# Performance work log

Measured on AMD Instinct MI355X. Metric: run time of the kernel, lower is better.

## Reference

```python
import jax, jax.numpy as jnp
import numpy as np

H, W, C = 64, 64, 64
B = 64
N_HEADS = 4
CONV_FILTERS = 64
BASIS_DIM = 16


def get_spatial_basis(h, w, d):
    half_d = d // 2
    basis = np.zeros((h, w, d), dtype=np.float32)
    div = np.exp(np.arange(0, half_d, 2, dtype=np.float32) * -np.log(100.0) / half_d)
    h_grid = np.expand_dims(np.arange(0, h, dtype=np.float32), 1)
    w_grid = np.expand_dims(np.arange(0, w, dtype=np.float32), 1)
    basis[:, :, 0:half_d:2] = np.sin(h_grid * div)[:, np.newaxis, :]
    basis[:, :, 1:half_d:2] = np.cos(h_grid * div)[:, np.newaxis, :]
    basis[:, :, half_d::2] = np.sin(w_grid * div)[np.newaxis, :, :]
    basis[:, :, half_d + 1::2] = np.cos(w_grid * div)[np.newaxis, :, :]
    return basis


def setup_inputs() -> dict:
    key = jax.random.key(0)
    ks = jax.random.split(key, 8)
    feat_in = C + BASIS_DIM  # 80 input channels for 1x1 convs
    return {
        "image": jax.random.normal(ks[0], (B, H, W, C), jnp.float32),
        "state1": jax.random.normal(ks[1], (B, 512), jnp.float32),
        "state2": jax.random.normal(ks[2], (B, 512), jnp.float32),
        "extra": jax.random.normal(ks[3], (B, 256), jnp.float32),
        "Wq": jax.random.normal(ks[4], (1024, CONV_FILTERS), jnp.float32) * 0.03,
        "bq": jnp.zeros((CONV_FILTERS,), jnp.float32),
        "Wk": jax.random.normal(ks[5], (feat_in, CONV_FILTERS), jnp.float32) * 0.1,
        "bk": jnp.zeros((CONV_FILTERS,), jnp.float32),
        "Wv": jax.random.normal(ks[6], (feat_in, CONV_FILTERS), jnp.float32) * 0.1,
        "bv": jnp.zeros((CONV_FILTERS,), jnp.float32),
        "spatial_basis": jnp.asarray(get_spatial_basis(H, W, BASIS_DIM)),
    }


def reference(image, state1, state2, extra, Wq, bq, Wk, bk, Wv, bv, spatial_basis):
    b, h, w, _ = image.shape
    nh = N_HEADS
    cf = Wq.shape[1]
    dph = cf // nh  # depth per head

    # concat image with tiled spatial basis -> [B,h,w,C+basis_dim]
    sb = jnp.broadcast_to(spatial_basis[None], (b,) + spatial_basis.shape)
    feats = jnp.concatenate([image, sb], axis=-1)

    # combiner over network-state tensors, then Dense query
    state = jnp.concatenate([state1, state2], axis=-1)  # [B,1024]
    q = state @ Wq + bq                                 # [B,cf]

    # 1x1 convs == per-pixel dense projections
    keys = feats @ Wk + bk    # [B,h,w,cf]
    vals = feats @ Wv + bv    # [B,h,w,cf]

    qh = q.reshape(b, nh, dph)
    kh = keys.reshape(b, h * w, nh, dph)
    vh = vals.reshape(b, h * w, nh, dph)

    # per-head dot scores over spatial positions, softmax over positions
    scores = jnp.einsum('bnd,bpnd->bpn', qh, kh)        # [B,hw,nh]
    attn = jax.nn.softmax(scores, axis=1)
    mean_attn = attn.mean(axis=-1).reshape(b, h, w)

    # weighted sum of values over spatial positions -> [B,cf]
    pooled = jnp.einsum('bpn,bpnd->bnd', attn, vh).reshape(b, cf)

    out = jnp.concatenate([pooled, extra], axis=-1)
    return out, mean_attn
```

## Files before the change

kernel.cpp:

```cpp
#include <hip/hip_runtime.h>
#include <hip/hip_bf16.h>

#define BATCH 64
#define HW    4096
#define PT    128
#define NS    32
#define FT_ST 136

#define FT_BASE  0
#define EST_BASE 10880
#define PR_BASE  13056
#define RED_BASE 15616
#define SMEM_TOT 15680

typedef unsigned int u32;
typedef unsigned short u16;
typedef __attribute__((ext_vector_type(8))) short bf16x8;
typedef __attribute__((ext_vector_type(4))) float f32x4;

__device__ __forceinline__ float bf2f(u16 h) { return __uint_as_float(((u32)h) << 16); }
__device__ __forceinline__ u32 f2bf(float x) {
  u32 b = __float_as_uint(x);
  return (b + 0x7fffu + ((b >> 16) & 1u)) >> 16;
}
__device__ __forceinline__ u32 pkbf(float lo, float hi) { return f2bf(lo) | (f2bf(hi) << 16); }

template<bool F32>
__device__ __forceinline__ float ld(const void* p, size_t i) {
  if (F32) return ((const float*)p)[i];
  return bf2f(((const u16*)p)[i]);
}
template<bool F32>
__device__ __forceinline__ void st(void* p, size_t i, float v) {
  if (F32) ((float*)p)[i] = v;
  else     ((__hip_bfloat16*)p)[i] = __float2bfloat16(v);
}

__device__ __forceinline__ bool detect_f32(const u16* __restrict__ image) {
  u16 h = image[(threadIdx.x & 63) * 2];
  u32 e = (h >> 7) & 0xFFu;
  unsigned long long m = __ballot(e >= 0x86u);
  return __popcll(m) >= 8;
}

template<bool F32>
__device__ void k1_body(const void* state1, const void* state2, const void* Wq, const void* bq,
                        const void* Wk, const void* bk, u16* weffbt, float* cb,
                        float* stt, float* qp, float* q) {
  const int b = blockIdx.x, tid = threadIdx.x;
  for (int i = tid; i < 512; i += 256) {
    stt[i]       = ld<F32>(state1, (size_t)b * 512 + i);
    stt[512 + i] = ld<F32>(state2, (size_t)b * 512 + i);
  }
  u32* wz = (u32*)(weffbt + (size_t)b * 1664);
  for (int i = tid; i < 832; i += 256) wz[i] = 0u;
  __syncthreads();
  {
    const int j = tid & 63, g = tid >> 6, i0 = g * 256;
    float a = 0.f;
#pragma unroll 8
    for (int i = 0; i < 256; ++i) a += stt[i0 + i] * ld<F32>(Wq, (size_t)(i0 + i) * 64 + j);
    qp[g * 64 + j] = a;
  }
  __syncthreads();
  if (tid < 64) q[tid] = qp[tid] + qp[64 + tid] + qp[128 + tid] + qp[192 + tid] + ld<F32>(bq, tid);
  __syncthreads();
  for (int t = tid; t < 320; t += 256) {
    const int c = t >> 2, n = t & 3;
    float a = 0.f;
#pragma unroll
    for (int d = 0; d < 16; ++d) a += ld<F32>(Wk, (size_t)c * 64 + n * 16 + d) * q[n * 16 + d];
    weffbt[(size_t)b * 1664 + n * 104 + c] = (u16)f2bf(a);
  }
  if (tid < 4) {
    float a = 0.f;
#pragma unroll
    for (int d = 0; d < 16; ++d) a += ld<F32>(bk, tid * 16 + d) * q[tid * 16 + d];
    cb[b * 4 + tid] = a;
  }
}

__global__ __launch_bounds__(256) void k1_prep(
    const void* image, const void* state1, const void* state2, const void* Wq, const void* bq,
    const void* Wk, const void* bk, u16* weffbt, float* cb) {
  __shared__ float stt[1024];
  __shared__ float qp[256];
  __shared__ float q[64];
  if (detect_f32((const u16*)image))
       k1_body<true >(state1, state2, Wq, bq, Wk, bk, weffbt, cb, stt, qp, q);
  else k1_body<false>(state1, state2, Wq, bq, Wk, bk, weffbt, cb, stt, qp, q);
}

__global__ __launch_bounds__(256, 4) void k2_main(
    const void* __restrict__ image, const void* __restrict__ basis,
    const float* __restrict__ cb, const u16* __restrict__ weffbt,
    u16* __restrict__ e_buf, float* __restrict__ m_blk, float* __restrict__ sum_blk,
    float* __restrict__ fpool_part) {
  __shared__ __align__(16) u16 smem[SMEM_TOT];
  float* redf  = (float*)(smem + RED_BASE);
  float* red2f = (float*)(smem + RED_BASE + 32);

  const int tid = threadIdx.x;
  const int b = blockIdx.x & 63, s = blockIdx.x >> 6;
  const int bs = b * NS + s;
  const int wave = tid >> 6, lane = tid & 63;
  const int m = lane & 15, q = lane >> 4;
  const bool isf32 = detect_f32((const u16*)image);

  if (isf32) {
    const float4* img4 = (const float4*)image + ((size_t)(b * HW + s * PT)) * 16;
#pragma unroll
    for (int i = 0; i < 4; ++i) {
      const int fidx = i * 256 + tid;
      const int pq = fidx >> 4, c4 = fidx & 15;
      float4 v0 = img4[(pq * 2) * 16 + c4];
      float4 v1 = img4[(pq * 2 + 1) * 16 + c4];
      *(u32*)&smem[FT_BASE + (c4 * 4 + 0) * FT_ST + pq * 2] = pkbf(v0.x, v1.x);
      *(u32*)&smem[FT_BASE + (c4 * 4 + 1) * FT_ST + pq * 2] = pkbf(v0.y, v1.y);
      *(u32*)&smem[FT_BASE + (c4 * 4 + 2) * FT_ST + pq * 2] = pkbf(v0.z, v1.z);
      *(u32*)&smem[FT_BASE + (c4 * 4 + 3) * FT_ST + pq * 2] = pkbf(v0.w, v1.w);
    }
    const float4* bas4 = (const float4*)basis + (size_t)(s * PT) * 4;
    {
      const int pq = tid >> 2, c4 = tid & 3;
      float4 v0 = bas4[(pq * 2) * 4 + c4];
      float4 v1 = bas4[(pq * 2 + 1) * 4 + c4];
      *(u32*)&smem[FT_BASE + (64 + c4 * 4 + 0) * FT_ST + pq * 2] = pkbf(v0.x, v1.x);
      *(u32*)&smem[FT_BASE + (64 + c4 * 4 + 1) * FT_ST + pq * 2] = pkbf(v0.y, v1.y);
      *(u32*)&smem[FT_BASE + (64 + c4 * 4 + 2) * FT_ST + pq * 2] = pkbf(v0.z, v1.z);
      *(u32*)&smem[FT_BASE + (64 + c4 * 4 + 3) * FT_ST + pq * 2] = pkbf(v0.w, v1.w);
    }
  } else {
    const uint4* img4 = (const uint4*)image + ((size_t)(b * HW + s * PT)) * 4;
    {
      const int pq = tid >> 2, c8 = tid & 3;
      uint4 u0 = img4[(pq * 2) * 4 + c8];
      uint4 u1 = img4[(pq * 2 + 1) * 4 + c8];
      const u32 w0[4] = {u0.x, u0.y, u0.z, u0.w};
      const u32 w1[4] = {u1.x, u1.y, u1.z, u1.w};
#pragma unroll
      for (int k = 0; k < 4; ++k) {
        *(u32*)&smem[FT_BASE + (c8 * 8 + 2 * k) * FT_ST + pq * 2]     = (w0[k] & 0xffffu) | (w1[k] << 16);
        *(u32*)&smem[FT_BASE + (c8 * 8 + 2 * k + 1) * FT_ST + pq * 2] = (w0[k] >> 16) | (w1[k] & 0xffff0000u);
      }
    }
    const uint4* bas4 = (const uint4*)basis + (size_t)(s * PT) * 2;
    if (tid < 128) {
      const int pq = tid >> 1, c8 = tid & 1;
      uint4 u0 = bas4[(pq * 2) * 2 + c8];
      uint4 u1 = bas4[(pq * 2 + 1) * 2 + c8];
      const u32 w0[4] = {u0.x, u0.y, u0.z, u0.w};
      const u32 w1[4] = {u1.x, u1.y, u1.z, u1.w};
#pragma unroll
      for (int k = 0; k < 4; ++k) {
        *(u32*)&smem[FT_BASE + (64 + c8 * 8 + 2 * k) * FT_ST + pq * 2]     = (w0[k] & 0xffffu) | (w1[k] << 16);
        *(u32*)&smem[FT_BASE + (64 + c8 * 8 + 2 * k + 1) * FT_ST + pq * 2] = (w0[k] >> 16) | (w1[k] & 0xffff0000u);
      }
    }
  }

  bf16x8 bfr[3];
  {
    const u16* wrow = weffbt + (size_t)b * 1664 + m * 104;
#pragma unroll
    for (int s3 = 0; s3 < 3; ++s3) bfr[s3] = *(const bf16x8*)&wrow[s3 * 32 + q * 8];
  }
  f32x4 accS[2];
  {
    const float ci = (m < 4) ? cb[b * 4 + m] : 0.f;
#pragma unroll
    for (int t = 0; t < 2; ++t) { accS[t][0] = ci; accS[t][1] = ci; accS[t][2] = ci; accS[t][3] = ci; }
#pragma unroll
    for (int t = 0; t < 2; ++t) {
      const int p = s * PT + (wave * 2 + t) * 16 + m;
#pragma unroll
      for (int s3 = 0; s3 < 3; ++s3) {
        bf16x8 a;
        if (isf32) {
          float4 v0, v1;
          if (s3 < 2) {
            const float4* ip = (const float4*)image + ((size_t)b * HW + p) * 16 + s3 * 8 + q * 2;
            v0 = ip[0]; v1 = ip[1];
          } else if (q < 2) {
            const float4* bp = (const float4*)basis + (size_t)p * 4 + q * 2;
            v0 = bp[0]; v1 = bp[1];
          } else { v0 = make_float4(0, 0, 0, 0); v1 = v0; }
          u32 aw[4] = {pkbf(v0.x, v0.y), pkbf(v0.z, v0.w), pkbf(v1.x, v1.y), pkbf(v1.z, v1.w)};
          a = *(const bf16x8*)aw;
        } else {
          if (s3 < 2) a = *(const bf16x8*)&((const u16*)image)[((size_t)b * HW + p) * 64 + s3 * 32 + q * 8];
          else if (q < 2) a = *(const bf16x8*)&((const u16*)basis)[(size_t)p * 16 + q * 8];
          else { u32 z[4] = {0, 0, 0, 0}; a = *(const bf16x8*)z; }
        }
        accS[t] = __builtin_amdgcn_mfma_f32_16x16x32_bf16(a, bfr[s3], accS[t], 0, 0, 0);
      }
    }
  }
  {
    float mx = accS[0][0];
#pragma unroll
    for (int t = 0; t < 2; ++t)
#pragma unroll
      for (int r = 0; r < 4; ++r) mx = fmaxf(mx, accS[t][r]);
    mx = fmaxf(mx, __shfl_xor(mx, 16, 64));
    mx = fmaxf(mx, __shfl_xor(mx, 32, 64));
    if (lane < 4) redf[wave * 4 + lane] = mx;
  }
  __syncthreads();

  float bmv;
  {
    const int hh = m & 3;
    bmv = fmaxf(fmaxf(redf[hh], redf[4 + hh]), fmaxf(redf[8 + hh], redf[12 + hh]));
  }
  {
    float ss = 0.f;
#pragma unroll
    for (int t = 0; t < 2; ++t) {
      const int T = wave * 2 + t;
#pragma unroll
      for (int r = 0; r < 4; ++r) {
        float e = __expf(accS[t][r] - bmv);
        u32 eb = f2bf(e);
        ss += bf2f((u16)eb);
        if (m < 4) smem[EST_BASE + m * FT_ST + T * 16 + q * 4 + r] = (u16)eb;
      }
    }
    ss += __shfl_xor(ss, 16, 64);
    ss += __shfl_xor(ss, 32, 64);
    if (lane < 4) red2f[wave * 4 + lane] = ss;
  }
  __syncthreads();

  if (tid < 4) {
    const int hh = tid;
    m_blk[bs * 4 + hh] = fmaxf(fmaxf(redf[hh], redf[4 + hh]), fmaxf(redf[8 + hh], redf[12 + hh]));
    sum_blk[bs * 4 + hh] = red2f[hh] + red2f[4 + hh] + red2f[8 + hh] + red2f[12 + hh];
  }
  {
    const int n = tid >> 6, pp = tid & 63;
    u32 v = *(const u32*)&smem[EST_BASE + n * FT_ST + pp * 2];
    ((u32*)e_buf)[((size_t)(b * 4 + n)) * 2048 + s * 64 + pp] = v;
  }
  {
    bf16x8 ap = *(const bf16x8*)&smem[EST_BASE + m * FT_ST + wave * 32 + q * 8];
    f32x4 accP[5];
#pragma unroll
    for (int T = 0; T < 5; ++T) { accP[T][0] = 0; accP[T][1] = 0; accP[T][2] = 0; accP[T][3] = 0; }
#pragma unroll
    for (int T = 0; T < 5; ++T) {
      bf16x8 bp = *(const bf16x8*)&smem[FT_BASE + (T * 16 + m) * FT_ST + wave * 32 + q * 8];
      accP[T] = __builtin_amdgcn_mfma_f32_16x16x32_bf16(ap, bp, accP[T], 0, 0, 0);
    }
    if (lane < 16) {
      float* pr = (float*)(smem + PR_BASE);
#pragma unroll
      for (int T = 0; T < 5; ++T)
#pragma unroll
        for (int r = 0; r < 4; ++r)
          pr[((wave * 5 + T) * 4 + r) * 16 + lane] = accP[T][r];
    }
  }
  __syncthreads();
  {
    const float* pr = (const float*)(smem + PR_BASE);
    for (int t = tid; t < 320; t += 256) {
      const int n = t / 80, c = t - n * 80;
      const int tile = c >> 4, cc = c & 15;
      float a = 0.f;
#pragma unroll
      for (int w = 0; w < 4; ++w) a += pr[((w * 5 + tile) * 4 + n) * 16 + cc];
      fpool_part[(size_t)bs * 320 + t] = a;
    }
  }
}

template<bool F32>
__device__ void k34_body(const float* m_blk, const float* sum_blk, const u16* e_buf,
                         const float* fpool_part, const void* Wv, const void* bv,
                         const void* extra, void* out, float* esc, float* fp) {
  const int tid = threadIdx.x;
  const int b = blockIdx.x & 63, s16 = blockIdx.x >> 6;
  if (tid < 4) {
    float M = -3.4e38f;
#pragma unroll
    for (int sp = 0; sp < NS; ++sp) M = fmaxf(M, m_blk[(b * NS + sp) * 4 + tid]);
    float den = 0.f;
#pragma unroll
    for (int sp = 0; sp < NS; ++sp)
      den += __expf(m_blk[(b * NS + sp) * 4 + tid] - M) * sum_blk[(b * NS + sp) * 4 + tid];
    float rd = 1.0f / den;
#pragma unroll
    for (int sp = 0; sp < NS; ++sp)
      esc[sp * 4 + tid] = __expf(m_blk[(b * NS + sp) * 4 + tid] - M) * rd;
  }
  __syncthreads();
  {
    const int gpos = s16 * 256 + tid;
    const int s32 = gpos >> 7;
    float mean = 0.f;
#pragma unroll
    for (int n = 0; n < 4; ++n)
      mean += bf2f(e_buf[(size_t)(b * 4 + n) * HW + gpos]) * esc[s32 * 4 + n];
    st<F32>(out, (size_t)BATCH * 320 + (size_t)b * HW + gpos, 0.25f * mean);
  }
  if (s16 == 0) {
    for (int idx = tid; idx < 320; idx += 256) {
      const int n2 = idx / 80;
      float a = 0.f;
#pragma unroll
      for (int sp = 0; sp < NS; ++sp)
        a += esc[sp * 4 + n2] * fpool_part[(size_t)(b * NS + sp) * 320 + idx];
      fp[idx] = a;
    }
    __syncthreads();
    if (tid < 64) {
      const int n = tid >> 4;
      float dot = 0.f;
#pragma unroll
      for (int c = 0; c < 80; ++c) dot += fp[n * 80 + c] * ld<F32>(Wv, (size_t)c * 64 + tid);
      st<F32>(out, (size_t)b * 320 + tid, dot + ld<F32>(bv, tid));
    }
    st<F32>(out, (size_t)b * 320 + 64 + tid, ld<F32>(extra, (size_t)b * 256 + tid));
  }
}

__global__ __launch_bounds__(256) void k34_out(
    const void* image, const float* m_blk, const float* sum_blk, const u16* e_buf,
    const float* fpool_part, const void* Wv, const void* bv, const void* extra, void* out) {
  __shared__ float esc[NS * 4];
  __shared__ float fp[320];
  if (detect_f32((const u16*)image))
       k34_body<true >(m_blk, sum_blk, e_buf, fpool_part, Wv, bv, extra, out, esc, fp);
  else k34_body<false>(m_blk, sum_blk, e_buf, fpool_part, Wv, bv, extra, out, esc, fp);
}

extern "C" void kernel_launch(void* const* d_in, const int* in_sizes, int n_in,
                              void* d_out, int out_size, void* d_ws, size_t ws_size,
                              hipStream_t stream) {
  (void)in_sizes; (void)n_in; (void)out_size; (void)ws_size;
  const void* image  = d_in[0];
  const void* state1 = d_in[1];
  const void* state2 = d_in[2];
  const void* extra  = d_in[3];
  const void* Wq = d_in[4];
  const void* bq = d_in[5];
  const void* Wk = d_in[6];
  const void* bk = d_in[7];
  const void* Wv = d_in[8];
  const void* bv = d_in[9];
  const void* basis = d_in[10];

  float* ws         = (float*)d_ws;
  float* cb         = ws;
  float* m_blk      = ws + 256;
  float* sum_blk    = ws + 8448;
  float* fpool_part = ws + 16640;
  u16*   weffbt     = (u16*)(ws + 672000);
  u16*   e_buf      = (u16*)(ws + 725248);

  k1_prep<<<dim3(BATCH), dim3(256), 0, stream>>>(image, state1, state2, Wq, bq, Wk, bk, weffbt, cb);
  k2_main<<<dim3(BATCH * NS), dim3(256), 0, stream>>>(image, basis, cb, weffbt,
                                                      e_buf, m_blk, sum_blk, fpool_part);
  k34_out<<<dim3(BATCH * 16), dim3(256), 0, stream>>>(image, m_blk, sum_blk, e_buf,
                                                      fpool_part, Wv, bv, extra, d_out);
}
```

Baseline: 139.5 us.

## Reuse staged LDS features for score MFMA and swizzle LDS layout

The score MFMA operands are now read from the transposed, bf16-packed feature tile in LDS instead of being reloaded from global memory, with a barrier added so the tile is complete before use. The LDS layout gets an XOR swizzle on position indices to reduce bank conflicts, applied consistently to the writes, the score reads and the pooling reads. The bf16 staging path is also widened to two iterations, which appears to fix previously incomplete image staging. Reading scores from LDS costs extra 16-bit LDS loads and an extra synchronization, in exchange for removing a duplicate global read and f32-to-bf16 conversion.

New measurement: 131.7 us. 1.06x faster.

```diff
diff --git a/kernel.cpp b/kernel.cpp
--- a/kernel.cpp
+++ b/kernel.cpp
@@ -42,6 +42,8 @@
   unsigned long long m = __ballot(e >= 0x86u);
   return __popcll(m) >= 8;
 }
+
+__device__ __forceinline__ int swz(int c) { return ((c >> 3) & 3) << 3; }
 
 template<bool F32>
 __device__ void k1_body(const void* state1, const void* state2, const void* Wq, const void* bq,
@@ -113,58 +115,65 @@
     for (int i = 0; i < 4; ++i) {
       const int fidx = i * 256 + tid;
       const int pq = fidx >> 4, c4 = fidx & 15;
+      const int ps = (pq * 2) ^ (((c4 >> 1) & 3) << 3);
       float4 v0 = img4[(pq * 2) * 16 + c4];
       float4 v1 = img4[(pq * 2 + 1) * 16 + c4];
-      *(u32*)&smem[FT_BASE + (c4 * 4 + 0) * FT_ST + pq * 2] = pkbf(v0.x, v1.x);
-      *(u32*)&smem[FT_BASE + (c4 * 4 + 1) * FT_ST + pq * 2] = pkbf(v0.y, v1.y);
-      *(u32*)&smem[FT_BASE + (c4 * 4 + 2) * FT_ST + pq * 2] = pkbf(v0.z, v1.z);
-      *(u32*)&smem[FT_BASE + (c4 * 4 + 3) * FT_ST + pq * 2] = pkbf(v0.w, v1.w);
+      *(u32*)&smem[FT_BASE + (c4 * 4 + 0) * FT_ST + ps] = pkbf(v0.x, v1.x);
+      *(u32*)&smem[FT_BASE + (c4 * 4 + 1) * FT_ST + ps] = pkbf(v0.y, v1.y);
+      *(u32*)&smem[FT_BASE + (c4 * 4 + 2) * FT_ST + ps] = pkbf(v0.z, v1.z);
+      *(u32*)&smem[FT_BASE + (c4 * 4 + 3) * FT_ST + ps] = pkbf(v0.w, v1.w);
     }
     const float4* bas4 = (const float4*)basis + (size_t)(s * PT) * 4;
     {
       const int pq = tid >> 2, c4 = tid & 3;
+      const int ps = (pq * 2) ^ (((c4 >> 1) & 3) << 3);
       float4 v0 = bas4[(pq * 2) * 4 + c4];
       float4 v1 = bas4[(pq * 2 + 1) * 4 + c4];
-      *(u32*)&smem[FT_BASE + (64 + c4 * 4 + 0) * FT_ST + pq * 2] = pkbf(v0.x, v1.x);
-      *(u32*)&smem[FT_BASE + (64 + c4 * 4 + 1) * FT_ST + pq * 2] = pkbf(v0.y, v1.y);
-      *(u32*)&smem[FT_BASE + (64 + c4 * 4 + 2) * FT_ST + pq * 2] = pkbf(v0.z, v1.z);
-      *(u32*)&smem[FT_BASE + (64 + c4 * 4 + 3) * FT_ST + pq * 2] = pkbf(v0.w, v1.w);
+      *(u32*)&smem[FT_BASE + (64 + c4 * 4 + 0) * FT_ST + ps] = pkbf(v0.x, v1.x);
+      *(u32*)&smem[FT_BASE + (64 + c4 * 4 + 1) * FT_ST + ps] = pkbf(v0.y, v1.y);
+      *(u32*)&smem[FT_BASE + (64 + c4 * 4 + 2) * FT_ST + ps] = pkbf(v0.z, v1.z);
+      *(u32*)&smem[FT_BASE + (64 + c4 * 4 + 3) * FT_ST + ps] = pkbf(v0.w, v1.w);
     }
   } else {
-    const uint4* img4 = (const uint4*)image + ((size_t)(b * HW + s * PT)) * 4;
-    {
-      const int pq = tid >> 2, c8 = tid & 3;
-      uint4 u0 = img4[(pq * 2) * 4 + c8];
-      uint4 u1 = img4[(pq * 2 + 1) * 4 + c8];
+    const uint4* img4 = (const uint4*)image + ((size_t)(b * HW + s * PT)) * 8;
+#pragma unroll
+    for (int i = 0; i < 2; ++i) {
+      const int fidx = i * 256 + tid;
+      const int pq = fidx >> 3, c8 = fidx & 7;
+      const int ps = (pq * 2) ^ ((c8 & 3) << 3);
+      uint4 u0 = img4[(pq * 2) * 8 + c8];
+      uint4 u1 = img4[(pq * 2 + 1) * 8 + c8];
       const u32 w0[4] = {u0.x, u0.y, u0.z, u0.w};
       const u32 w1[4] = {u1.x, u1.y, u1.z, u1.w};
 #pragma unroll
       for (int k = 0; k < 4; ++k) {
-        *(u32*)&smem[FT_BASE + (c8 * 8 + 2 * k) * FT_ST + pq * 2]     = (w0[k] & 0xffffu) | (w1[k] << 16);
-        *(u32*)&smem[FT_BASE + (c8 * 8 + 2 * k + 1) * FT_ST + pq * 2] = (w0[k] >> 16) | (w1[k] & 0xffff0000u);
+        *(u32*)&smem[FT_BASE + (c8 * 8 + 2 * k) * FT_ST + ps]     = (w0[k] & 0xffffu) | (w1[k] << 16);
+        *(u32*)&smem[FT_BASE + (c8 * 8 + 2 * k + 1) * FT_ST + ps] = (w0[k] >> 16) | (w1[k] & 0xffff0000u);
       }
     }
     const uint4* bas4 = (const uint4*)basis + (size_t)(s * PT) * 2;
     if (tid < 128) {
       const int pq = tid >> 1, c8 = tid & 1;
+      const int ps = (pq * 2) ^ ((c8 & 3) << 3);
       uint4 u0 = bas4[(pq * 2) * 2 + c8];
       uint4 u1 = bas4[(pq * 2 + 1) * 2 + c8];
       const u32 w0[4] = {u0.x, u0.y, u0.z, u0.w};
       const u32 w1[4] = {u1.x, u1.y, u1.z, u1.w};
 #pragma unroll
       for (int k = 0; k < 4; ++k) {
-        *(u32*)&smem[FT_BASE + (64 + c8 * 8 + 2 * k) * FT_ST + pq * 2]     = (w0[k] & 0xffffu) | (w1[k] << 16);
-        *(u32*)&smem[FT_BASE + (64 + c8 * 8 + 2 * k + 1) * FT_ST + pq * 2] = (w0[k] >> 16) | (w1[k] & 0xffff0000u);
+        *(u32*)&smem[FT_BASE + (64 + c8 * 8 + 2 * k) * FT_ST + ps]     = (w0[k] & 0xffffu) | (w1[k] << 16);
+        *(u32*)&smem[FT_BASE + (64 + c8 * 8 + 2 * k + 1) * FT_ST + ps] = (w0[k] >> 16) | (w1[k] & 0xffff0000u);
       }
     }
   }
-
   bf16x8 bfr[3];
   {
     const u16* wrow = weffbt + (size_t)b * 1664 + m * 104;
 #pragma unroll
     for (int s3 = 0; s3 < 3; ++s3) bfr[s3] = *(const bf16x8*)&wrow[s3 * 32 + q * 8];
   }
+  __syncthreads();
+
   f32x4 accS[2];
   {
     const float ci = (m < 4) ? cb[b * 4 + m] : 0.f;
@@ -172,27 +181,23 @@
     for (int t = 0; t < 2; ++t) { accS[t][0] = ci; accS[t][1] = ci; accS[t][2] = ci; accS[t][3] = ci; }
 #pragma unroll
     for (int t = 0; t < 2; ++t) {
-      const int p = s * PT + (wave * 2 + t) * 16 + m;
+      const int pos = (wave * 2 + t) * 16 + m;
 #pragma unroll
       for (int s3 = 0; s3 < 3; ++s3) {
-        bf16x8 a;
-        if (isf32) {
-          float4 v0, v1;
-          if (s3 < 2) {
-            const float4* ip = (const float4*)image + ((size_t)b * HW + p) * 16 + s3 * 8 + q * 2;
-            v0 = ip[0]; v1 = ip[1];
-          } else if (q < 2) {
-            const float4* bp = (const float4*)basis + (size_t)p * 4 + q * 2;
-            v0 = bp[0]; v1 = bp[1];
-          } else { v0 = make_float4(0, 0, 0, 0); v1 = v0; }
-          u32 aw[4] = {pkbf(v0.x, v0.y), pkbf(v0.z, v0.w), pkbf(v1.x, v1.y), pkbf(v1.z, v1.w)};
-          a = *(const bf16x8*)aw;
+        u32 aw[4];
+        if (s3 == 2 && q >= 2) {
+          aw[0] = aw[1] = aw[2] = aw[3] = 0u;
         } else {
-          if (s3 < 2) a = *(const bf16x8*)&((const u16*)image)[((size_t)b * HW + p) * 64 + s3 * 32 + q * 8];
-          else if (q < 2) a = *(const bf16x8*)&((const u16*)basis)[(size_t)p * 16 + q * 8];
-          else { u32 z[4] = {0, 0, 0, 0}; a = *(const bf16x8*)z; }
+#pragma unroll
+          for (int jp = 0; jp < 4; ++jp) {
+            const int c0 = s3 * 32 + q * 8 + jp * 2;
+            const int ps = pos ^ swz(c0);
+            u32 lo = smem[FT_BASE + c0 * FT_ST + ps];
+            u32 hi = smem[FT_BASE + (c0 + 1) * FT_ST + ps];
+            aw[jp] = lo | (hi << 16);
+          }
         }
-        accS[t] = __builtin_amdgcn_mfma_f32_16x16x32_bf16(a, bfr[s3], accS[t], 0, 0, 0);
+        accS[t] = __builtin_amdgcn_mfma_f32_16x16x32_bf16(*(const bf16x8*)aw, bfr[s3], accS[t], 0, 0, 0);
       }
     }
   }
@@ -249,7 +254,9 @@
     for (int T = 0; T < 5; ++T) { accP[T][0] = 0; accP[T][1] = 0; accP[T][2] = 0; accP[T][3] = 0; }
 #pragma unroll
     for (int T = 0; T < 5; ++T) {
-      bf16x8 bp = *(const bf16x8*)&smem[FT_BASE + (T * 16 + m) * FT_ST + wave * 32 + q * 8];
+      const int c = T * 16 + m;
+      const int g = (wave * 32 + q * 8) ^ swz(c);
+      bf16x8 bp = *(const bf16x8*)&smem[FT_BASE + c * FT_ST + g];
       accP[T] = __builtin_amdgcn_mfma_f32_16x16x32_bf16(ap, bp, accP[T], 0, 0, 0);
     }
     if (lane < 16) {
```
